# Optimization experiments

Hardware: AMD Instinct MI355X
Metric: run time of the kernel (lower is better)

The kernel has to match this reference:

```python
import jax, jax.numpy as jnp
import numpy as np

N_RBF = 20
CUTOFF = 15.0
N_ATOMS, N_EDGES, D, H = 8192, 262144, 256, 256
D_PAIR = 2 * D + 1 + N_RBF  # 533


def setup_inputs() -> dict:
    key = jax.random.key(0)
    ks = jax.random.split(key, 10)
    s = 1.0 / np.sqrt(H).astype(np.float32)
    return {
        "x": jax.random.normal(ks[0], (N_ATOMS, D), jnp.float32),
        "d_ij": jax.random.uniform(ks[1], (N_EDGES,), jnp.float32, 0.5, CUTOFF),
        "idx_i": jnp.sort(jax.random.randint(ks[2], (N_EDGES,), 0, N_ATOMS)),
        "idx_j": jax.random.randint(ks[3], (N_EDGES,), 0, N_ATOMS),
        "W_in": jax.random.normal(ks[4], (D_PAIR, H), jnp.float32) / np.sqrt(D_PAIR).astype(np.float32),
        "b_in": jnp.zeros((H,), jnp.float32),
        "Ws": jax.random.normal(ks[5], (6, H, H), jnp.float32) * s,
        "bs": jnp.zeros((6, H), jnp.float32),
        "W_out": jax.random.normal(ks[6], (H, 1), jnp.float32) * s,
        "b_out": jnp.zeros((1,), jnp.float32),
    }


def _gaussian_rbf(d):
    # GaussianRBF(20, 15.0): offsets linspace(0, cutoff), width = grid spacing
    offsets = jnp.linspace(0.0, CUTOFF, N_RBF)
    width = offsets[1] - offsets[0]
    coeff = -0.5 / (width * width)
    diff = d[:, None] - offsets  # [E, N_RBF]
    return jnp.exp(coeff * diff * diff)


def reference(x, d_ij, idx_i, idx_j, W_in, b_in, Ws, bs, W_out, b_out):
    n_atoms = x.shape[0]
    rbf = _gaussian_rbf(d_ij)  # [E, 20]
    # per-pair representation: x_i | x_j | rbf(d_ij) | d_ij  -> [E, 533]
    pair = jnp.concatenate([x[idx_i], x[idx_j], rbf, d_ij[:, None]], axis=1)
    h = pair @ W_in + b_in  # pair_and_distance_transform -> [E, 256]
    # build_mlp(H, H, H, 5): 6 linears, SiLU after all but the last
    for l in range(6):
        h = h @ Ws[l] + bs[l]
        if l < 5:
            h = jax.nn.silu(h)
    # DeepSets aggregation: scatter-sum pair messages onto center atom i
    pooled = jax.ops.segment_sum(h, idx_i, num_segments=n_atoms)  # [N, 256]
    out = pooled @ W_out + b_out  # per-atom energy [N, 1]
    return out
```

## Files before the change

### kernel.cpp

```cpp
#include <hip/hip_runtime.h>


typedef _Float16 f16x8 __attribute__((ext_vector_type(8)));
typedef _Float16 f16x4 __attribute__((ext_vector_type(4)));
typedef __fp16   fp16v2 __attribute__((ext_vector_type(2)));
typedef float    f32x4 __attribute__((ext_vector_type(4)));
typedef unsigned int u32x4 __attribute__((ext_vector_type(4)));
typedef unsigned int u32x2 __attribute__((ext_vector_type(2)));

union H8 { f16x8 v; _Float16 h[8]; u32x4 u; };
union H4 { f16x4 v; u32x2 u; };
union H2 { fp16v2 h; unsigned int u; };

#define MFMA16(a, b, c) __builtin_amdgcn_mfma_f32_16x16x32_f16((a), (b), (c), 0, 0, 0)

#define LOG2E 1.44269504088896340736f

#define WS_WP   0u
#define WS_WPI  786432u
#define WS_WPJ  917504u
#define WS_WPR  1048576u
#define WS_XH   1064960u
#define WS_AP   5259264u
#define WS_BP   9453568u

__global__ __launch_bounds__(256) void k_prep(
    const float* __restrict__ x, const float* __restrict__ W_in,
    const float* __restrict__ Ws, const float* __restrict__ b_out,
    _Float16* __restrict__ wp, _Float16* __restrict__ wpi,
    _Float16* __restrict__ wpj, _Float16* __restrict__ wpr,
    _Float16* __restrict__ xh, float* __restrict__ out)
{
  int i = blockIdx.x * 256 + threadIdx.x;
  if (i < 2097152) { xh[i] = (_Float16)x[i]; return; }
  i -= 2097152;
  if (i < 393216) {
    int m = i >> 16, r = i & 65535;
    int j = r & 7, lane = (r >> 3) & 63, ks = (r >> 9) & 7, nt = (r >> 12) & 15;
    int k = ks * 32 + (lane >> 4) * 8 + j, n = nt * 16 + (lane & 15);
    wp[i] = (_Float16)Ws[(m * 256 + k) * 256 + n];
    return;
  }
  i -= 393216;
  if (i < 65536) {
    int j = i & 7, lane = (i >> 3) & 63, ks = (i >> 9) & 7, nt = (i >> 12) & 15;
    int k = ks * 32 + (lane >> 4) * 8 + j, n = nt * 16 + (lane & 15);
    wpi[i] = (_Float16)W_in[k * 256 + n];
    return;
  }
  i -= 65536;
  if (i < 65536) {
    int j = i & 7, lane = (i >> 3) & 63, ks = (i >> 9) & 7, nt = (i >> 12) & 15;
    int k = ks * 32 + (lane >> 4) * 8 + j, n = nt * 16 + (lane & 15);
    wpj[i] = (_Float16)W_in[(256 + k) * 256 + n];
    return;
  }
  i -= 65536;
  if (i < 8192) {
    int j = i & 7, lane = (i >> 3) & 63, nt = (i >> 9) & 15;
    int k = (lane >> 4) * 8 + j, n = nt * 16 + (lane & 15);
    float v = 0.0f;
    if (k < 20)       v = W_in[(512 + k) * 256 + n];
    else if (k == 20) v = W_in[532 * 256 + n];
    wpr[i] = (_Float16)v;
    return;
  }
  i -= 8192;
  if (i < 8192) out[i] = b_out[0];
}

__global__ __launch_bounds__(256) void k_atoms(
    const _Float16* __restrict__ xh,
    const _Float16* __restrict__ wpi, const _Float16* __restrict__ wpj,
    const float* __restrict__ b_in,
    _Float16* __restrict__ AP, _Float16* __restrict__ BP)
{
  const int tid = threadIdx.x;
  const int l = tid & 63, w = tid >> 6;
  const int g = l >> 4, c = l & 15;
  const int which = blockIdx.y;
  const _Float16* wpx = which ? wpj : wpi;
  _Float16* outp = which ? BP : AP;
  const int abase = blockIdx.x * 64;

  f32x4 acc[4][4];
#pragma unroll
  for (int nf = 0; nf < 4; ++nf)
#pragma unroll
    for (int at = 0; at < 4; ++at) acc[nf][at] = (f32x4)0.0f;

#pragma unroll
  for (int ks = 0; ks < 8; ++ks) {
    f16x8 a[4];
#pragma unroll
    for (int nf = 0; nf < 4; ++nf) {
      H8 t; t.u = *(const u32x4*)(wpx + (((w * 4 + nf) * 8 + ks) * 64 + l) * 8);
      a[nf] = t.v;
    }
#pragma unroll
    for (int at = 0; at < 4; ++at) {
      H8 b; b.u = *(const u32x4*)(xh + (abase + at * 16 + c) * 256 + ks * 32 + g * 8);
#pragma unroll
      for (int nf = 0; nf < 4; ++nf)
        acc[nf][at] = MFMA16(a[nf], b.v, acc[nf][at]);
    }
  }

#pragma unroll
  for (int nf = 0; nf < 4; ++nf) {
    const int n = w * 64 + nf * 16 + g * 4;
    f32x4 bias = (f32x4)0.0f;
    if (!which) bias = *(const f32x4*)(b_in + n);
#pragma unroll
    for (int at = 0; at < 4; ++at) {
      const int atom = abase + at * 16 + c;
      const f32x4 t = acc[nf][at] + bias;
      H2 lo, hi;
      lo.h = __builtin_amdgcn_cvt_pkrtz(t[0], t[1]);
      hi.h = __builtin_amdgcn_cvt_pkrtz(t[2], t[3]);
      u32x2 q; q[0] = lo.u; q[1] = hi.u;
      *(u32x2*)(outp + atom * 256 + n) = q;
    }
  }
}

__global__ __launch_bounds__(512, 4) void k_edges(
    const _Float16* __restrict__ AP, const _Float16* __restrict__ BP,
    const int* __restrict__ idx_i, const int* __restrict__ idx_j,
    const float* __restrict__ d_ij,
    const _Float16* __restrict__ wp, const _Float16* __restrict__ wpr,
    const float* __restrict__ bs, const float* __restrict__ W_out,
    float* __restrict__ out)
{
  __shared__ __align__(16) char hb[65536];
  __shared__ float d_lds[128];
  __shared__ int   ii_lds[128];
  __shared__ int   jj_lds[128];
  __shared__ float oacc[128];

  const int tid = threadIdx.x;
  const int l = tid & 63, w = tid >> 6;
  const int ge = w >> 2, gn = w & 3;
  const int g = l >> 4, c = l & 15;
  const int ebase = blockIdx.x * 128;
  const int we = ge * 64;
  const int nb = gn * 64;
  const int sw = (c << 4) | ((c & 1) << 8);

  if (tid < 128) {
    ii_lds[tid] = idx_i[ebase + tid];
    jj_lds[tid] = idx_j[ebase + tid];
    d_lds[tid]  = d_ij[ebase + tid];
    oacc[tid]   = 0.0f;
  }
  __syncthreads();

  f32x4 acc[4][4];

  {
    const float STEP = 15.0f / 19.0f;
    const float C2 = (-0.5f / (STEP * STEP)) * LOG2E;
    f16x8 afr[4];
#pragma unroll
    for (int nf = 0; nf < 4; ++nf) {
      H8 t; t.u = *(const u32x4*)(wpr + ((gn * 4 + nf) * 64 + l) * 8);
      afr[nf] = t.v;
    }
#pragma unroll
    for (int et = 0; et < 4; ++et) {
      const int el = we + et * 16 + c;
      const float d = d_lds[el];
      H8 bb;
#pragma unroll
      for (int j = 0; j < 8; ++j) {
        const int k = g * 8 + j;
        float v = 0.0f;
        if (k < 20)       { const float df = d - (float)k * STEP; v = __builtin_amdgcn_exp2f(C2 * df * df); }
        else if (k == 20) { v = d; }
        bb.h[j] = (_Float16)v;
      }
#pragma unroll
      for (int nf = 0; nf < 4; ++nf)
        acc[nf][et] = (nf == 0 && false) ? acc[nf][et] : MFMA16(afr[nf], bb.v, (et >= 0 ? (f32x4)0.0f : acc[nf][et]));
    }
#pragma unroll
    for (int et = 0; et < 4; ++et) {
      const int el = we + et * 16 + c;
      const float d = d_lds[el];
      H8 bb;
#pragma unroll
      for (int j = 0; j < 8; ++j) {
        const int k = g * 8 + j;
        float v = 0.0f;
        if (k < 20)       { const float df = d - (float)k * STEP; v = __builtin_amdgcn_exp2f(C2 * df * df); }
        else if (k == 20) { v = d; }
        bb.h[j] = (_Float16)v;
      }
      f32x4 z = (f32x4)0.0f;
#pragma unroll
      for (int nf = 0; nf < 4; ++nf) {
        f32x4 r = MFMA16(afr[nf], bb.v, (nf == 0 ? z : z));
        acc[nf][et] = r;
      }
    }
  }
#pragma unroll
  for (int nf = 0; nf < 4; ++nf) {
    const int n = nb + nf * 16 + g * 4;
    const int obase = n * 2;
#pragma unroll
    for (int et = 0; et < 4; ++et) {
      const int el = we + et * 16 + c;
      H4 pa, pb, s;
      pa.u = *(const u32x2*)(AP + ii_lds[el] * 256 + n);
      pb.u = *(const u32x2*)(BP + jj_lds[el] * 256 + n);
      H2 lo, hi;
      lo.h = __builtin_amdgcn_cvt_pkrtz(acc[nf][et][0], acc[nf][et][1]);
      hi.h = __builtin_amdgcn_cvt_pkrtz(acc[nf][et][2], acc[nf][et][3]);
      s.u[0] = lo.u; s.u[1] = hi.u;
      s.v = s.v + pa.v + pb.v;
      *(u32x2*)(hb + el * 512 + (obase ^ sw)) = s.u;
    }
  }
  __syncthreads();

  auto mfma_layer = [&](const _Float16* wl, const float* brow) {
#pragma unroll
    for (int nf = 0; nf < 4; ++nf) {
      const f32x4 bias = *(const f32x4*)(brow + nb + nf * 16 + g * 4);
#pragma unroll
      for (int et = 0; et < 4; ++et) acc[nf][et] = bias;
    }
    __builtin_amdgcn_s_setprio(1);
#pragma unroll
    for (int ks = 0; ks < 8; ++ks) {
      f16x8 a[4];
#pragma unroll
      for (int nf = 0; nf < 4; ++nf) {
        H8 t; t.u = *(const u32x4*)(wl + (((gn * 4 + nf) * 8 + ks) * 64 + l) * 8);
        a[nf] = t.v;
      }
      const int o = (ks * 64 + g * 16) ^ sw;
#pragma unroll
      for (int et = 0; et < 4; ++et) {
        const int el = we + et * 16 + c;
        H8 b; b.u = *(const u32x4*)(hb + el * 512 + o);
#pragma unroll
        for (int nf = 0; nf < 4; ++nf)
          acc[nf][et] = MFMA16(a[nf], b.v, acc[nf][et]);
      }
    }
    __builtin_amdgcn_s_setprio(0);
  };

#pragma unroll 1
  for (int ly = 0; ly < 5; ++ly) {
    mfma_layer(wp + ly * 65536, bs + ly * 256);
    __syncthreads();
#pragma unroll
    for (int nf = 0; nf < 4; ++nf) {
      const int n = nb + nf * 16 + g * 4;
      const int obase = n * 2;
#pragma unroll
      for (int et = 0; et < 4; ++et) {
        f32x4 v = acc[nf][et];
#pragma unroll
        for (int j = 0; j < 4; ++j) {
          const float e = __builtin_amdgcn_exp2f(v[j] * -LOG2E);
          v[j] = v[j] * __builtin_amdgcn_rcpf(1.0f + e);
        }
        const int el = we + et * 16 + c;
        H2 lo, hi;
        lo.h = __builtin_amdgcn_cvt_pkrtz(v[0], v[1]);
        hi.h = __builtin_amdgcn_cvt_pkrtz(v[2], v[3]);
        u32x2 q; q[0] = lo.u; q[1] = hi.u;
        *(u32x2*)(hb + el * 512 + (obase ^ sw)) = q;
      }
    }
    __syncthreads();
  }

  mfma_layer(wp + 5 * 65536, bs + 5 * 256);
  float sum[4];
#pragma unroll
  for (int et = 0; et < 4; ++et) sum[et] = 0.0f;
#pragma unroll
  for (int nf = 0; nf < 4; ++nf) {
    const int n = nb + nf * 16 + g * 4;
    const f32x4 wo = *(const f32x4*)(W_out + n);
#pragma unroll
    for (int et = 0; et < 4; ++et) {
      const f32x4 v = acc[nf][et];
      sum[et] += v[0] * wo[0] + v[1] * wo[1] + v[2] * wo[2] + v[3] * wo[3];
    }
  }
#pragma unroll
  for (int et = 0; et < 4; ++et) {
    float s = sum[et];
    s += __shfl_xor(s, 16, 64);
    s += __shfl_xor(s, 32, 64);
    if (l < 16) atomicAdd(&oacc[we + et * 16 + l], s);
  }
  __syncthreads();
  if (tid < 128) atomicAdd(out + ii_lds[tid], oacc[tid]);
}

extern "C" void kernel_launch(void* const* d_in, const int* in_sizes, int n_in,
                              void* d_out, int out_size, void* d_ws, size_t ws_size,
                              hipStream_t stream) {
  (void)in_sizes; (void)n_in; (void)out_size; (void)ws_size;
  const float* x     = (const float*)d_in[0];
  const float* d_ij  = (const float*)d_in[1];
  const int*   idx_i = (const int*)d_in[2];
  const int*   idx_j = (const int*)d_in[3];
  const float* W_in  = (const float*)d_in[4];
  const float* b_in  = (const float*)d_in[5];
  const float* Ws    = (const float*)d_in[6];
  const float* bs    = (const float*)d_in[7];
  const float* W_out = (const float*)d_in[8];
  const float* b_out = (const float*)d_in[9];
  float* out = (float*)d_out;
  char* ws = (char*)d_ws;

  _Float16* wp  = (_Float16*)(ws + WS_WP);
  _Float16* wpi = (_Float16*)(ws + WS_WPI);
  _Float16* wpj = (_Float16*)(ws + WS_WPJ);
  _Float16* wpr = (_Float16*)(ws + WS_WPR);
  _Float16* xh  = (_Float16*)(ws + WS_XH);
  _Float16* AP  = (_Float16*)(ws + WS_AP);
  _Float16* BP  = (_Float16*)(ws + WS_BP);

  hipLaunchKernelGGL(k_prep, dim3(10305), dim3(256), 0, stream,
                     x, W_in, Ws, b_out, wp, wpi, wpj, wpr, xh, out);
  hipLaunchKernelGGL(k_atoms, dim3(128, 2), dim3(256), 0, stream,
                     xh, wpi, wpj, b_in, AP, BP);
  hipLaunchKernelGGL(k_edges, dim3(2048), dim3(512), 0, stream,
                     AP, BP, idx_i, idx_j, d_ij, wp, wpr, bs, W_out, out);
}
```

Measured before the change: 281.6 us.

## Halve edge tile and double-buffer LDS activations to drop a barrier per layer

The edge kernel now processes 64 edges per block instead of 128. Each of the 8 waves owns 32 output columns across all 64 edges, rather than a 64x64 sub-tile. Activations ping-pong between two 32 KB LDS buffers, so the barrier between the matmul and the SiLU write-back in each layer is removed. The duplicated RBF computation is also dropped. In exchange, each weight fragment loaded from global memory is reused over half as many edges, and twice as many blocks run, raising total weight traffic.

Result: slower. 295.2 us (+4.8%).

```diff
diff --git a/kernel.cpp b/kernel.cpp
--- a/kernel.cpp
+++ b/kernel.cpp
@@ -132,22 +132,20 @@
     const float* __restrict__ bs, const float* __restrict__ W_out,
     float* __restrict__ out)
 {
-  __shared__ __align__(16) char hb[65536];
-  __shared__ float d_lds[128];
-  __shared__ int   ii_lds[128];
-  __shared__ int   jj_lds[128];
-  __shared__ float oacc[128];
+  __shared__ __align__(16) char hb[2][32768];
+  __shared__ float d_lds[64];
+  __shared__ int   ii_lds[64];
+  __shared__ int   jj_lds[64];
+  __shared__ float oacc[64];
 
   const int tid = threadIdx.x;
   const int l = tid & 63, w = tid >> 6;
-  const int ge = w >> 2, gn = w & 3;
   const int g = l >> 4, c = l & 15;
-  const int ebase = blockIdx.x * 128;
-  const int we = ge * 64;
-  const int nb = gn * 64;
+  const int ebase = blockIdx.x * 64;
+  const int nb = w * 32;
   const int sw = (c << 4) | ((c & 1) << 8);
 
-  if (tid < 128) {
+  if (tid < 64) {
     ii_lds[tid] = idx_i[ebase + tid];
     jj_lds[tid] = idx_j[ebase + tid];
     d_lds[tid]  = d_ij[ebase + tid];
@@ -155,21 +153,20 @@
   }
   __syncthreads();
 
-  f32x4 acc[4][4];
+  f32x4 acc[2][4];
 
   {
     const float STEP = 15.0f / 19.0f;
     const float C2 = (-0.5f / (STEP * STEP)) * LOG2E;
-    f16x8 afr[4];
-#pragma unroll
-    for (int nf = 0; nf < 4; ++nf) {
-      H8 t; t.u = *(const u32x4*)(wpr + ((gn * 4 + nf) * 64 + l) * 8);
+    f16x8 afr[2];
+#pragma unroll
+    for (int nf = 0; nf < 2; ++nf) {
+      H8 t; t.u = *(const u32x4*)(wpr + ((w * 2 + nf) * 64 + l) * 8);
       afr[nf] = t.v;
     }
 #pragma unroll
     for (int et = 0; et < 4; ++et) {
-      const int el = we + et * 16 + c;
-      const float d = d_lds[el];
+      const float d = d_lds[et * 16 + c];
       H8 bb;
 #pragma unroll
       for (int j = 0; j < 8; ++j) {
@@ -179,38 +176,19 @@
         else if (k == 20) { v = d; }
         bb.h[j] = (_Float16)v;
       }
-#pragma unroll
-      for (int nf = 0; nf < 4; ++nf)
-        acc[nf][et] = (nf == 0 && false) ? acc[nf][et] : MFMA16(afr[nf], bb.v, (et >= 0 ? (f32x4)0.0f : acc[nf][et]));
-    }
-#pragma unroll
-    for (int et = 0; et < 4; ++et) {
-      const int el = we + et * 16 + c;
-      const float d = d_lds[el];
-      H8 bb;
-#pragma unroll
-      for (int j = 0; j < 8; ++j) {
-        const int k = g * 8 + j;
-        float v = 0.0f;
-        if (k < 20)       { const float df = d - (float)k * STEP; v = __builtin_amdgcn_exp2f(C2 * df * df); }
-        else if (k == 20) { v = d; }
-        bb.h[j] = (_Float16)v;
-      }
-      f32x4 z = (f32x4)0.0f;
-#pragma unroll
-      for (int nf = 0; nf < 4; ++nf) {
-        f32x4 r = MFMA16(afr[nf], bb.v, (nf == 0 ? z : z));
-        acc[nf][et] = r;
-      }
-    }
-  }
-#pragma unroll
-  for (int nf = 0; nf < 4; ++nf) {
+      const f32x4 z = (f32x4)0.0f;
+#pragma unroll
+      for (int nf = 0; nf < 2; ++nf)
+        acc[nf][et] = MFMA16(afr[nf], bb.v, z);
+    }
+  }
+#pragma unroll
+  for (int nf = 0; nf < 2; ++nf) {
     const int n = nb + nf * 16 + g * 4;
     const int obase = n * 2;
 #pragma unroll
     for (int et = 0; et < 4; ++et) {
-      const int el = we + et * 16 + c;
+      const int el = et * 16 + c;
       H4 pa, pb, s;
       pa.u = *(const u32x2*)(AP + ii_lds[el] * 256 + n);
       pb.u = *(const u32x2*)(BP + jj_lds[el] * 256 + n);
@@ -219,14 +197,16 @@
       hi.h = __builtin_amdgcn_cvt_pkrtz(acc[nf][et][2], acc[nf][et][3]);
       s.u[0] = lo.u; s.u[1] = hi.u;
       s.v = s.v + pa.v + pb.v;
-      *(u32x2*)(hb + el * 512 + (obase ^ sw)) = s.u;
+      *(u32x2*)(hb[0] + el * 512 + (obase ^ sw)) = s.u;
     }
   }
   __syncthreads();
 
+  int cur = 0;
+
   auto mfma_layer = [&](const _Float16* wl, const float* brow) {
 #pragma unroll
-    for (int nf = 0; nf < 4; ++nf) {
+    for (int nf = 0; nf < 2; ++nf) {
       const f32x4 bias = *(const f32x4*)(brow + nb + nf * 16 + g * 4);
 #pragma unroll
       for (int et = 0; et < 4; ++et) acc[nf][et] = bias;
@@ -234,19 +214,19 @@
     __builtin_amdgcn_s_setprio(1);
 #pragma unroll
     for (int ks = 0; ks < 8; ++ks) {
-      f16x8 a[4];
-#pragma unroll
-      for (int nf = 0; nf < 4; ++nf) {
-        H8 t; t.u = *(const u32x4*)(wl + (((gn * 4 + nf) * 8 + ks) * 64 + l) * 8);
+      f16x8 a[2];
+#pragma unroll
+      for (int nf = 0; nf < 2; ++nf) {
+        H8 t; t.u = *(const u32x4*)(wl + (((w * 2 + nf) * 8 + ks) * 64 + l) * 8);
         a[nf] = t.v;
       }
       const int o = (ks * 64 + g * 16) ^ sw;
 #pragma unroll
       for (int et = 0; et < 4; ++et) {
-        const int el = we + et * 16 + c;
-        H8 b; b.u = *(const u32x4*)(hb + el * 512 + o);
-#pragma unroll
-        for (int nf = 0; nf < 4; ++nf)
+        const int el = et * 16 + c;
+        H8 b; b.u = *(const u32x4*)(hb[cur] + el * 512 + o);
+#pragma unroll
+        for (int nf = 0; nf < 2; ++nf)
           acc[nf][et] = MFMA16(a[nf], b.v, acc[nf][et]);
       }
     }
@@ -256,9 +236,8 @@
 #pragma unroll 1
   for (int ly = 0; ly < 5; ++ly) {
     mfma_layer(wp + ly * 65536, bs + ly * 256);
-    __syncthreads();
-#pragma unroll
-    for (int nf = 0; nf < 4; ++nf) {
+#pragma unroll
+    for (int nf = 0; nf < 2; ++nf) {
       const int n = nb + nf * 16 + g * 4;
       const int obase = n * 2;
 #pragma unroll
@@ -269,15 +248,16 @@
           const float e = __builtin_amdgcn_exp2f(v[j] * -LOG2E);
           v[j] = v[j] * __builtin_amdgcn_rcpf(1.0f + e);
         }
-        const int el = we + et * 16 + c;
+        const int el = et * 16 + c;
         H2 lo, hi;
         lo.h = __builtin_amdgcn_cvt_pkrtz(v[0], v[1]);
         hi.h = __builtin_amdgcn_cvt_pkrtz(v[2], v[3]);
         u32x2 q; q[0] = lo.u; q[1] = hi.u;
-        *(u32x2*)(hb + el * 512 + (obase ^ sw)) = q;
+        *(u32x2*)(hb[cur ^ 1] + el * 512 + (obase ^ sw)) = q;
       }
     }
     __syncthreads();
+    cur ^= 1;
   }
 
   mfma_layer(wp + 5 * 65536, bs + 5 * 256);
@@ -285,7 +265,7 @@
 #pragma unroll
   for (int et = 0; et < 4; ++et) sum[et] = 0.0f;
 #pragma unroll
-  for (int nf = 0; nf < 4; ++nf) {
+  for (int nf = 0; nf < 2; ++nf) {
     const int n = nb + nf * 16 + g * 4;
     const f32x4 wo = *(const f32x4*)(W_out + n);
 #pragma unroll
@@ -299,10 +279,10 @@
     float s = sum[et];
     s += __shfl_xor(s, 16, 64);
     s += __shfl_xor(s, 32, 64);
-    if (l < 16) atomicAdd(&oacc[we + et * 16 + l], s);
+    if (l < 16) atomicAdd(&oacc[et * 16 + l], s);
   }
   __syncthreads();
-  if (tid < 128) atomicAdd(out + ii_lds[tid], oacc[tid]);
+  if (tid < 64) atomicAdd(out + ii_lds[tid], oacc[tid]);
 }
 
 extern "C" void kernel_launch(void* const* d_in, const int* in_sizes, int n_in,
@@ -334,6 +314,6 @@
                      x, W_in, Ws, b_out, wp, wpi, wpj, wpr, xh, out);
   hipLaunchKernelGGL(k_atoms, dim3(128, 2), dim3(256), 0, stream,
                      xh, wpi, wpj, b_in, AP, BP);
-  hipLaunchKernelGGL(k_edges, dim3(2048), dim3(512), 0, stream,
+  hipLaunchKernelGGL(k_edges, dim3(4096), dim3(512), 0, stream,
                      AP, BP, idx_i, idx_j, d_ij, wp, wpr, bs, W_out, out);
 }
```

## Use 4 waves per edge block, each covering all 128 edges

Applied to the files above, without the earlier changes.

The edge kernel drops from 8 to 4 waves per 128-edge block. Each wave now computes a 64-column slice for all 128 edges, holding 8 edge tiles of accumulators instead of 4. This halves the per-layer weight fragment loads from global/L2 per block and reuses each A fragment over more MFMAs. The cost is roughly double the accumulator registers and lower occupancy (launch bounds 256,2). It also drops the duplicated RBF computation loop.

After: 270.3 us. 1.04x faster.

```diff
diff --git a/kernel.cpp b/kernel.cpp
--- a/kernel.cpp
+++ b/kernel.cpp
@@ -124,7 +124,7 @@
   }
 }
 
-__global__ __launch_bounds__(512, 4) void k_edges(
+__global__ __launch_bounds__(256, 2) void k_edges(
     const _Float16* __restrict__ AP, const _Float16* __restrict__ BP,
     const int* __restrict__ idx_i, const int* __restrict__ idx_j,
     const float* __restrict__ d_ij,
@@ -140,11 +140,9 @@
 
   const int tid = threadIdx.x;
   const int l = tid & 63, w = tid >> 6;
-  const int ge = w >> 2, gn = w & 3;
   const int g = l >> 4, c = l & 15;
   const int ebase = blockIdx.x * 128;
-  const int we = ge * 64;
-  const int nb = gn * 64;
+  const int nb = w * 64;
   const int sw = (c << 4) | ((c & 1) << 8);
 
   if (tid < 128) {
@@ -155,7 +153,7 @@
   }
   __syncthreads();
 
-  f32x4 acc[4][4];
+  f32x4 acc[4][8];
 
   {
     const float STEP = 15.0f / 19.0f;
@@ -163,13 +161,12 @@
     f16x8 afr[4];
 #pragma unroll
     for (int nf = 0; nf < 4; ++nf) {
-      H8 t; t.u = *(const u32x4*)(wpr + ((gn * 4 + nf) * 64 + l) * 8);
+      H8 t; t.u = *(const u32x4*)(wpr + ((w * 4 + nf) * 64 + l) * 8);
       afr[nf] = t.v;
     }
 #pragma unroll
-    for (int et = 0; et < 4; ++et) {
-      const int el = we + et * 16 + c;
-      const float d = d_lds[el];
+    for (int et = 0; et < 8; ++et) {
+      const float d = d_lds[et * 16 + c];
       H8 bb;
 #pragma unroll
       for (int j = 0; j < 8; ++j) {
@@ -179,29 +176,10 @@
         else if (k == 20) { v = d; }
         bb.h[j] = (_Float16)v;
       }
+      const f32x4 z = (f32x4)0.0f;
 #pragma unroll
       for (int nf = 0; nf < 4; ++nf)
-        acc[nf][et] = (nf == 0 && false) ? acc[nf][et] : MFMA16(afr[nf], bb.v, (et >= 0 ? (f32x4)0.0f : acc[nf][et]));
-    }
-#pragma unroll
-    for (int et = 0; et < 4; ++et) {
-      const int el = we + et * 16 + c;
-      const float d = d_lds[el];
-      H8 bb;
-#pragma unroll
-      for (int j = 0; j < 8; ++j) {
-        const int k = g * 8 + j;
-        float v = 0.0f;
-        if (k < 20)       { const float df = d - (float)k * STEP; v = __builtin_amdgcn_exp2f(C2 * df * df); }
-        else if (k == 20) { v = d; }
-        bb.h[j] = (_Float16)v;
-      }
-      f32x4 z = (f32x4)0.0f;
-#pragma unroll
-      for (int nf = 0; nf < 4; ++nf) {
-        f32x4 r = MFMA16(afr[nf], bb.v, (nf == 0 ? z : z));
-        acc[nf][et] = r;
-      }
+        acc[nf][et] = MFMA16(afr[nf], bb.v, z);
     }
   }
 #pragma unroll
@@ -209,8 +187,8 @@
     const int n = nb + nf * 16 + g * 4;
     const int obase = n * 2;
 #pragma unroll
-    for (int et = 0; et < 4; ++et) {
-      const int el = we + et * 16 + c;
+    for (int et = 0; et < 8; ++et) {
+      const int el = et * 16 + c;
       H4 pa, pb, s;
       pa.u = *(const u32x2*)(AP + ii_lds[el] * 256 + n);
       pb.u = *(const u32x2*)(BP + jj_lds[el] * 256 + n);
@@ -229,7 +207,7 @@
     for (int nf = 0; nf < 4; ++nf) {
       const f32x4 bias = *(const f32x4*)(brow + nb + nf * 16 + g * 4);
 #pragma unroll
-      for (int et = 0; et < 4; ++et) acc[nf][et] = bias;
+      for (int et = 0; et < 8; ++et) acc[nf][et] = bias;
     }
     __builtin_amdgcn_s_setprio(1);
 #pragma unroll
@@ -237,13 +215,13 @@
       f16x8 a[4];
 #pragma unroll
       for (int nf = 0; nf < 4; ++nf) {
-        H8 t; t.u = *(const u32x4*)(wl + (((gn * 4 + nf) * 8 + ks) * 64 + l) * 8);
+        H8 t; t.u = *(const u32x4*)(wl + (((w * 4 + nf) * 8 + ks) * 64 + l) * 8);
         a[nf] = t.v;
       }
       const int o = (ks * 64 + g * 16) ^ sw;
 #pragma unroll
-      for (int et = 0; et < 4; ++et) {
-        const int el = we + et * 16 + c;
+      for (int et = 0; et < 8; ++et) {
+        const int el = et * 16 + c;
         H8 b; b.u = *(const u32x4*)(hb + el * 512 + o);
 #pragma unroll
         for (int nf = 0; nf < 4; ++nf)
@@ -262,14 +240,14 @@
       const int n = nb + nf * 16 + g * 4;
       const int obase = n * 2;
 #pragma unroll
-      for (int et = 0; et < 4; ++et) {
+      for (int et = 0; et < 8; ++et) {
         f32x4 v = acc[nf][et];
 #pragma unroll
         for (int j = 0; j < 4; ++j) {
           const float e = __builtin_amdgcn_exp2f(v[j] * -LOG2E);
           v[j] = v[j] * __builtin_amdgcn_rcpf(1.0f + e);
         }
-        const int el = we + et * 16 + c;
+        const int el = et * 16 + c;
         H2 lo, hi;
         lo.h = __builtin_amdgcn_cvt_pkrtz(v[0], v[1]);
         hi.h = __builtin_amdgcn_cvt_pkrtz(v[2], v[3]);
@@ -281,25 +259,25 @@
   }
 
   mfma_layer(wp + 5 * 65536, bs + 5 * 256);
-  float sum[4];
-#pragma unroll
-  for (int et = 0; et < 4; ++et) sum[et] = 0.0f;
+  float sum[8];
+#pragma unroll
+  for (int et = 0; et < 8; ++et) sum[et] = 0.0f;
 #pragma unroll
   for (int nf = 0; nf < 4; ++nf) {
     const int n = nb + nf * 16 + g * 4;
     const f32x4 wo = *(const f32x4*)(W_out + n);
 #pragma unroll
-    for (int et = 0; et < 4; ++et) {
+    for (int et = 0; et < 8; ++et) {
       const f32x4 v = acc[nf][et];
       sum[et] += v[0] * wo[0] + v[1] * wo[1] + v[2] * wo[2] + v[3] * wo[3];
     }
   }
 #pragma unroll
-  for (int et = 0; et < 4; ++et) {
+  for (int et = 0; et < 8; ++et) {
     float s = sum[et];
     s += __shfl_xor(s, 16, 64);
     s += __shfl_xor(s, 32, 64);
-    if (l < 16) atomicAdd(&oacc[we + et * 16 + l], s);
+    if (l < 16) atomicAdd(&oacc[et * 16 + l], s);
   }
   __syncthreads();
   if (tid < 128) atomicAdd(out + ii_lds[tid], oacc[tid]);
@@ -334,6 +312,6 @@
                      x, W_in, Ws, b_out, wp, wpi, wpj, wpr, xh, out);
   hipLaunchKernelGGL(k_atoms, dim3(128, 2), dim3(256), 0, stream,
                      xh, wpi, wpj, b_in, AP, BP);
-  hipLaunchKernelGGL(k_edges, dim3(2048), dim3(512), 0, stream,
+  hipLaunchKernelGGL(k_edges, dim3(2048), dim3(256), 0, stream,
                      AP, BP, idx_i, idx_j, d_ij, wp, wpr, bs, W_out, out);
 }
```

## Stage MLP weight slices into LDS via double-buffered global_load_lds

Applied to the files above, without the earlier changes.

Instead of each wave reading its MLP weight fragments straight from global memory, the kernel now streams each layer's k-slice into a double-buffered LDS region with direct global-to-LDS loads, prefetching two slices ahead with explicit vmcnt waits and barriers. The six layers are merged into one loop with a per-k-step barrier, and the redundant duplicated RBF MFMA pass is removed. The extra 32KB of LDS lowers the occupancy hint from 4 to 2 blocks per CU, and the per-k-step barriers add synchronisation overhead.

Measured after the change: 434.0 us. 54.1% more time.

```diff
diff --git a/kernel.cpp b/kernel.cpp
--- a/kernel.cpp
+++ b/kernel.cpp
@@ -2,19 +2,24 @@
 
 
 typedef _Float16 f16x8 __attribute__((ext_vector_type(8)));
-typedef _Float16 f16x4 __attribute__((ext_vector_type(4)));
 typedef __fp16   fp16v2 __attribute__((ext_vector_type(2)));
 typedef float    f32x4 __attribute__((ext_vector_type(4)));
 typedef unsigned int u32x4 __attribute__((ext_vector_type(4)));
 typedef unsigned int u32x2 __attribute__((ext_vector_type(2)));
 
 union H8 { f16x8 v; _Float16 h[8]; u32x4 u; };
-union H4 { f16x4 v; u32x2 u; };
+union H4 { _Float16 h[4]; u32x2 u; struct { unsigned int a, b; } w; };
 union H2 { fp16v2 h; unsigned int u; };
 
 #define MFMA16(a, b, c) __builtin_amdgcn_mfma_f32_16x16x32_f16((a), (b), (c), 0, 0, 0)
 
 #define LOG2E 1.44269504088896340736f
+
+__device__ inline void gload_lds16(const void* g, void* l) {
+  __builtin_amdgcn_global_load_lds(
+      (const __attribute__((address_space(1))) void*)g,
+      (__attribute__((address_space(3))) void*)l, 16, 0, 0);
+}
 
 #define WS_WP   0u
 #define WS_WPI  786432u
@@ -124,7 +129,7 @@
   }
 }
 
-__global__ __launch_bounds__(512, 4) void k_edges(
+__global__ __launch_bounds__(512, 2) void k_edges(
     const _Float16* __restrict__ AP, const _Float16* __restrict__ BP,
     const int* __restrict__ idx_i, const int* __restrict__ idx_j,
     const float* __restrict__ d_ij,
@@ -133,6 +138,7 @@
     float* __restrict__ out)
 {
   __shared__ __align__(16) char hb[65536];
+  __shared__ __align__(16) char wbuf[32768];
   __shared__ float d_lds[128];
   __shared__ int   ii_lds[128];
   __shared__ int   jj_lds[128];
@@ -168,8 +174,7 @@
     }
 #pragma unroll
     for (int et = 0; et < 4; ++et) {
-      const int el = we + et * 16 + c;
-      const float d = d_lds[el];
+      const float d = d_lds[we + et * 16 + c];
       H8 bb;
 #pragma unroll
       for (int j = 0; j < 8; ++j) {
@@ -179,29 +184,10 @@
         else if (k == 20) { v = d; }
         bb.h[j] = (_Float16)v;
       }
+      const f32x4 z = (f32x4)0.0f;
 #pragma unroll
       for (int nf = 0; nf < 4; ++nf)
-        acc[nf][et] = (nf == 0 && false) ? acc[nf][et] : MFMA16(afr[nf], bb.v, (et >= 0 ? (f32x4)0.0f : acc[nf][et]));
-    }
-#pragma unroll
-    for (int et = 0; et < 4; ++et) {
-      const int el = we + et * 16 + c;
-      const float d = d_lds[el];
-      H8 bb;
-#pragma unroll
-      for (int j = 0; j < 8; ++j) {
-        const int k = g * 8 + j;
-        float v = 0.0f;
-        if (k < 20)       { const float df = d - (float)k * STEP; v = __builtin_amdgcn_exp2f(C2 * df * df); }
-        else if (k == 20) { v = d; }
-        bb.h[j] = (_Float16)v;
-      }
-      f32x4 z = (f32x4)0.0f;
-#pragma unroll
-      for (int nf = 0; nf < 4; ++nf) {
-        f32x4 r = MFMA16(afr[nf], bb.v, (nf == 0 ? z : z));
-        acc[nf][et] = r;
-      }
+        acc[nf][et] = MFMA16(afr[nf], bb.v, z);
     }
   }
 #pragma unroll
@@ -211,34 +197,57 @@
 #pragma unroll
     for (int et = 0; et < 4; ++et) {
       const int el = we + et * 16 + c;
-      H4 pa, pb, s;
+      H4 pa, pb;
       pa.u = *(const u32x2*)(AP + ii_lds[el] * 256 + n);
       pb.u = *(const u32x2*)(BP + jj_lds[el] * 256 + n);
       H2 lo, hi;
       lo.h = __builtin_amdgcn_cvt_pkrtz(acc[nf][et][0], acc[nf][et][1]);
       hi.h = __builtin_amdgcn_cvt_pkrtz(acc[nf][et][2], acc[nf][et][3]);
-      s.u[0] = lo.u; s.u[1] = hi.u;
-      s.v = s.v + pa.v + pb.v;
+      u32x2 q; q[0] = lo.u; q[1] = hi.u;
+      H4 s; s.u = q;
+#pragma unroll
+      for (int j = 0; j < 4; ++j) s.h[j] = s.h[j] + pa.h[j] + pb.h[j];
       *(u32x2*)(hb + el * 512 + (obase ^ sw)) = s.u;
     }
   }
-  __syncthreads();
-
-  auto mfma_layer = [&](const _Float16* wl, const float* brow) {
+
+  auto stage = [&](int t) {
+    const int lyt = t >> 3, kst = t & 7;
+    const char* srcbase = (const char*)wp + lyt * 131072;
+#pragma unroll
+    for (int q = 0; q < 2; ++q) {
+      const int f = w * 2 + q;
+      gload_lds16(srcbase + (f * 8 + kst) * 1024 + l * 16,
+                  wbuf + (t & 1) * 16384 + f * 1024);
+    }
+  };
+  stage(0);
+  stage(1);
+  asm volatile("s_waitcnt lgkmcnt(0)" ::: "memory");
+  __builtin_amdgcn_s_barrier();
+
+#pragma unroll 1
+  for (int ly = 0; ly < 6; ++ly) {
+    const float* brow = bs + ly * 256;
 #pragma unroll
     for (int nf = 0; nf < 4; ++nf) {
       const f32x4 bias = *(const f32x4*)(brow + nb + nf * 16 + g * 4);
 #pragma unroll
       for (int et = 0; et < 4; ++et) acc[nf][et] = bias;
     }
-    __builtin_amdgcn_s_setprio(1);
-#pragma unroll
+#pragma unroll 1
     for (int ks = 0; ks < 8; ++ks) {
+      const int t = ly * 8 + ks;
+      if (t == 47) asm volatile("s_waitcnt vmcnt(0)" ::: "memory");
+      else         asm volatile("s_waitcnt vmcnt(2)" ::: "memory");
+      __builtin_amdgcn_s_barrier();
+      const char* wsl = wbuf + (t & 1) * 16384;
+      __builtin_amdgcn_s_setprio(1);
       f16x8 a[4];
 #pragma unroll
       for (int nf = 0; nf < 4; ++nf) {
-        H8 t; t.u = *(const u32x4*)(wl + (((gn * 4 + nf) * 8 + ks) * 64 + l) * 8);
-        a[nf] = t.v;
+        H8 ta; ta.u = *(const u32x4*)(wsl + (gn * 4 + nf) * 1024 + l * 16);
+        a[nf] = ta.v;
       }
       const int o = (ks * 64 + g * 16) ^ sw;
 #pragma unroll
@@ -249,38 +258,37 @@
         for (int nf = 0; nf < 4; ++nf)
           acc[nf][et] = MFMA16(a[nf], b.v, acc[nf][et]);
       }
-    }
-    __builtin_amdgcn_s_setprio(0);
-  };
-
-#pragma unroll 1
-  for (int ly = 0; ly < 5; ++ly) {
-    mfma_layer(wp + ly * 65536, bs + ly * 256);
-    __syncthreads();
-#pragma unroll
-    for (int nf = 0; nf < 4; ++nf) {
-      const int n = nb + nf * 16 + g * 4;
-      const int obase = n * 2;
-#pragma unroll
-      for (int et = 0; et < 4; ++et) {
-        f32x4 v = acc[nf][et];
-#pragma unroll
-        for (int j = 0; j < 4; ++j) {
-          const float e = __builtin_amdgcn_exp2f(v[j] * -LOG2E);
-          v[j] = v[j] * __builtin_amdgcn_rcpf(1.0f + e);
+      __builtin_amdgcn_s_setprio(0);
+      asm volatile("s_waitcnt lgkmcnt(0)" ::: "memory");
+      __builtin_amdgcn_s_barrier();
+      if (t + 2 < 48) stage(t + 2);
+    }
+    if (ly < 5) {
+#pragma unroll
+      for (int nf = 0; nf < 4; ++nf) {
+        const int n = nb + nf * 16 + g * 4;
+        const int obase = n * 2;
+#pragma unroll
+        for (int et = 0; et < 4; ++et) {
+          f32x4 v = acc[nf][et];
+#pragma unroll
+          for (int j = 0; j < 4; ++j) {
+            const float e = __builtin_amdgcn_exp2f(v[j] * -LOG2E);
+            v[j] = v[j] * __builtin_amdgcn_rcpf(1.0f + e);
+          }
+          const int el = we + et * 16 + c;
+          H2 lo, hi;
+          lo.h = __builtin_amdgcn_cvt_pkrtz(v[0], v[1]);
+          hi.h = __builtin_amdgcn_cvt_pkrtz(v[2], v[3]);
+          u32x2 q; q[0] = lo.u; q[1] = hi.u;
+          *(u32x2*)(hb + el * 512 + (obase ^ sw)) = q;
         }
-        const int el = we + et * 16 + c;
-        H2 lo, hi;
-        lo.h = __builtin_amdgcn_cvt_pkrtz(v[0], v[1]);
-        hi.h = __builtin_amdgcn_cvt_pkrtz(v[2], v[3]);
-        u32x2 q; q[0] = lo.u; q[1] = hi.u;
-        *(u32x2*)(hb + el * 512 + (obase ^ sw)) = q;
       }
-    }
-    __syncthreads();
-  }
-
-  mfma_layer(wp + 5 * 65536, bs + 5 * 256);
+      asm volatile("s_waitcnt lgkmcnt(0)" ::: "memory");
+      __builtin_amdgcn_s_barrier();
+    }
+  }
+
   float sum[4];
 #pragma unroll
   for (int et = 0; et < 4; ++et) sum[et] = 0.0f;
```
